# Kernel tuning notes

Measured on AMD Instinct MI355X. Metric: run time of the kernel, lower is better.

The kernel has to match this reference:

```python
import jax, jax.numpy as jnp
import numpy as np

C = 128          # channel_size
H = 2            # num_head
HD = C // H      # per-head dim = 64
SCALE = C ** 0.5 # note: module scales by sqrt(channel_size), not sqrt(head_dim)


def setup_inputs() -> dict:
    key = jax.random.key(0)
    k_x, k_w, k_b = jax.random.split(key, 3)
    x = jax.random.normal(k_x, (8, 64, 256, C), dtype=jnp.float32)
    # nn.Linear(C, 3C): weight [3C, C], bias [3C]; y = x @ W.T + b
    bound = 1.0 / np.sqrt(C)
    W_qkv = jax.random.uniform(k_w, (3 * C, C), dtype=jnp.float32, minval=-bound, maxval=bound)
    b_qkv = jax.random.uniform(k_b, (3 * C,), dtype=jnp.float32, minval=-bound, maxval=bound)
    return {"x": x, "W_qkv": W_qkv, "b_qkv": b_qkv}


def reference(x, W_qkv, b_qkv):
    b, l, g, _ = x.shape
    qkv = jnp.einsum('blgc,dc->blgd', x, W_qkv) + b_qkv        # [b,l,g,3C]
    # rearrange 'b l g (d h c) -> d b l h g c'
    qkv = qkv.reshape(b, l, g, 3, H, HD)
    qkv = jnp.transpose(qkv, (3, 0, 1, 4, 2, 5))               # [3,b,l,h,g,c]
    q, k, v = qkv[0], qkv[1], qkv[2]
    score = jnp.einsum('blhgc,blhkc->blhgk', q, k) / SCALE      # [b,l,h,g,g]
    score = jax.nn.softmax(score, axis=-1)
    out = jnp.einsum('blhgk,blhkc->blhgc', score, v)            # [b,l,h,g,c]
    # rearrange 'b l h g c -> b l g (h c)'
    out = jnp.transpose(out, (0, 1, 3, 2, 4)).reshape(b, l, g, H * HD)
    return out
```

## Files before the change

### kernel.cpp

```cpp
#include <hip/hip_runtime.h>
#include <hip/hip_bf16.h>


typedef __bf16 bf16x8 __attribute__((ext_vector_type(8)));
typedef float  f32x4  __attribute__((ext_vector_type(4)));
typedef float  f32x16 __attribute__((ext_vector_type(16)));

#define MFMA16(a, b, c) __builtin_amdgcn_mfma_f32_16x16x32_bf16((a), (b), (c), 0, 0, 0)
#define MFMA32(a, b, c) __builtin_amdgcn_mfma_f32_32x32x16_bf16((a), (b), (c), 0, 0, 0)

namespace dmsa {

constexpr int G  = 256;
constexpr int C  = 128;
constexpr int HD = 64;
constexpr float QSCALE = 1.4426950408889634f * 0.08838834764831845f;

__device__ __forceinline__ unsigned pack2(float a, float b) {
    union { __hip_bfloat162 h; unsigned u; } c;
    c.h = __float22bfloat162_rn(make_float2(a, b));
    return c.u;
}
__device__ __forceinline__ uint2 pack4(float a, float b, float c, float d) {
    uint2 r; r.x = pack2(a, b); r.y = pack2(c, d); return r;
}
__device__ __forceinline__ uint4 pack8(const float* p) {
    uint4 r;
    r.x = pack2(p[0], p[1]); r.y = pack2(p[2], p[3]);
    r.z = pack2(p[4], p[5]); r.w = pack2(p[6], p[7]);
    return r;
}
__device__ __forceinline__ bf16x8 lds8(const ushort* p) { return *(const bf16x8*)p; }
__device__ __forceinline__ bf16x8 ldg8(const ushort* p) { return *(const bf16x8*)p; }
__device__ __forceinline__ bf16x8 ld8f(const float* __restrict__ p) {
    float t[8];
    *(float4*)t       = *(const float4*)p;
    *(float4*)(t + 4) = *(const float4*)(p + 4);
    union { uint4 u; bf16x8 v; } c;
    c.u = pack8(t);
    return c.v;
}

__global__ void convw(const float* __restrict__ W, ushort* __restrict__ wbf) {
    int t = blockIdx.x * 256 + threadIdx.x;
    float tmp[8];
    const float* p = W + (size_t)t * 8;
    *(float4*)tmp       = *(const float4*)p;
    *(float4*)(tmp + 4) = *(const float4*)(p + 4);
    *(uint4*)(wbf + (size_t)t * 8) = pack8(tmp);
}

__global__ __launch_bounds__(256, 2)
void fused(const float* __restrict__ x, const ushort* __restrict__ wb,
           const float* __restrict__ bias, float* __restrict__ out)
{
    __shared__ ushort kc[G * 72];
    __shared__ ushort vc[HD * 264];

    const int tid = threadIdx.x, wv = tid >> 6, lane = tid & 63;
    const int l16 = lane & 15, quad = lane >> 4;
    const int l32 = lane & 31, hl = lane >> 5;

    const int b  = blockIdx.x;
    const int L  = ((b & 7) << 7) | (b >> 3);
    const int bl = L >> 1, h = L & 1;

    const float*  xr = x  + (size_t)bl * G * C;
    const ushort* Wq = wb + (size_t)(h * HD) * C;
    const ushort* Wk = wb + (size_t)(C + h * HD) * C;
    const ushort* Wv = wb + (size_t)(2 * C + h * HD) * C;

    const int r0 = wv * 64;
    const f32x4 z4 = {0.f, 0.f, 0.f, 0.f};

    bf16x8 xf[4][4];
    #pragma unroll
    for (int i = 0; i < 4; ++i)
        #pragma unroll
        for (int kk = 0; kk < 4; ++kk)
            xf[i][kk] = ld8f(xr + (size_t)(r0 + i * 16 + l16) * C + kk * 32 + quad * 8);

    f32x4 qacc[4][4];
    #pragma unroll
    for (int mi = 0; mi < 4; ++mi)
        #pragma unroll
        for (int ni = 0; ni < 4; ++ni) qacc[mi][ni] = z4;
    #pragma unroll
    for (int kk = 0; kk < 4; ++kk)
        #pragma unroll
        for (int mi = 0; mi < 4; ++mi) {
            bf16x8 a = ldg8(Wq + (size_t)(mi * 16 + l16) * C + kk * 32 + quad * 8);
            #pragma unroll
            for (int ni = 0; ni < 4; ++ni)
                qacc[mi][ni] = MFMA16(a, xf[ni][kk], qacc[mi][ni]);
        }
    ushort* qs = kc + r0 * 72;
    #pragma unroll
    for (int mi = 0; mi < 4; ++mi) {
        float4 bs = *(const float4*)(bias + h * HD + mi * 16 + quad * 4);
        #pragma unroll
        for (int ni = 0; ni < 4; ++ni)
            *(uint2*)(qs + (ni * 16 + l16) * 72 + mi * 16 + quad * 4) =
                pack4((qacc[mi][ni][0] + bs.x) * QSCALE,
                      (qacc[mi][ni][1] + bs.y) * QSCALE,
                      (qacc[mi][ni][2] + bs.z) * QSCALE,
                      (qacc[mi][ni][3] + bs.w) * QSCALE);
    }
    bf16x8 qf[2][4];
    #pragma unroll
    for (int ni = 0; ni < 2; ++ni)
        #pragma unroll
        for (int kk = 0; kk < 4; ++kk)
            qf[ni][kk] = lds8(qs + (ni * 32 + l32) * 72 + kk * 16 + hl * 8);

    {
        f32x4 kacc[4][4];
        #pragma unroll
        for (int mi = 0; mi < 4; ++mi)
            #pragma unroll
            for (int nt = 0; nt < 4; ++nt) kacc[mi][nt] = z4;
        #pragma unroll
        for (int kk = 0; kk < 4; ++kk)
            #pragma unroll
            for (int mi = 0; mi < 4; ++mi) {
                bf16x8 a = ldg8(Wk + (size_t)(mi * 16 + l16) * C + kk * 32 + quad * 8);
                #pragma unroll
                for (int nt = 0; nt < 4; ++nt)
                    kacc[mi][nt] = MFMA16(a, xf[nt][kk], kacc[mi][nt]);
            }
        #pragma unroll
        for (int mi = 0; mi < 4; ++mi) {
            float4 bs = *(const float4*)(bias + C + h * HD + mi * 16 + quad * 4);
            #pragma unroll
            for (int nt = 0; nt < 4; ++nt)
                *(uint2*)(kc + (r0 + nt * 16 + l16) * 72 + mi * 16 + quad * 4) =
                    pack4(kacc[mi][nt][0] + bs.x, kacc[mi][nt][1] + bs.y,
                          kacc[mi][nt][2] + bs.z, kacc[mi][nt][3] + bs.w);
        }
    }

    {
        f32x4 vacc[4][4];
        #pragma unroll
        for (int mt = 0; mt < 4; ++mt)
            #pragma unroll
            for (int nt = 0; nt < 4; ++nt) vacc[mt][nt] = z4;
        #pragma unroll
        for (int kk = 0; kk < 4; ++kk)
            #pragma unroll
            for (int nt = 0; nt < 4; ++nt) {
                bf16x8 bw = ldg8(Wv + (size_t)(nt * 16 + l16) * C + kk * 32 + quad * 8);
                #pragma unroll
                for (int mt = 0; mt < 4; ++mt)
                    vacc[mt][nt] = MFMA16(xf[mt][kk], bw, vacc[mt][nt]);
            }
        #pragma unroll
        for (int nt = 0; nt < 4; ++nt) {
            float bv = bias[2 * C + h * HD + nt * 16 + l16];
            #pragma unroll
            for (int mt = 0; mt < 4; ++mt)
                *(uint2*)(vc + (nt * 16 + l16) * 264 + r0 + mt * 16 + quad * 4) =
                    pack4(vacc[mt][nt][0] + bv, vacc[mt][nt][1] + bv,
                          vacc[mt][nt][2] + bv, vacc[mt][nt][3] + bv);
        }
    }

    __syncthreads();

    float lacc[2] = {0.f, 0.f};
    f32x16 oacc[2][2];
    #pragma unroll
    for (int mt = 0; mt < 2; ++mt)
        #pragma unroll
        for (int ni = 0; ni < 2; ++ni)
            #pragma unroll
            for (int r = 0; r < 16; ++r) oacc[mt][ni][r] = 0.f;

    #pragma unroll 2
    for (int sp = 0; sp < 8; ++sp) {
        const int g0 = sp * 32;

        bf16x8 kf[4];
        #pragma unroll
        for (int kk = 0; kk < 4; ++kk)
            kf[kk] = lds8(kc + (g0 + l32) * 72 + kk * 16 + hl * 8);
        bf16x8 vf[2][2];
        #pragma unroll
        for (int mt = 0; mt < 2; ++mt)
            #pragma unroll
            for (int ch = 0; ch < 2; ++ch)
                vf[mt][ch] = lds8(vc + (mt * 32 + l32) * 264 + g0 + ch * 16 + hl * 8);

        #pragma unroll
        for (int ni = 0; ni < 2; ++ni) {
            f32x16 s;
            #pragma unroll
            for (int r = 0; r < 16; ++r) s[r] = 0.f;
            __builtin_amdgcn_s_setprio(1);
            #pragma unroll
            for (int kk = 0; kk < 4; ++kk)
                s = MFMA32(kf[kk], qf[ni][kk], s);
            __builtin_amdgcn_s_setprio(0);

            float part = 0.f;
            #pragma unroll
            for (int r = 0; r < 16; ++r) {
                float p = exp2f(s[r]);
                s[r] = p;
                part += p;
            }
            lacc[ni] += part;

            #pragma unroll
            for (int ch = 0; ch < 2; ++ch) {
                unsigned p0a = pack2(s[8 * ch + 0], s[8 * ch + 1]);
                unsigned p0b = pack2(s[8 * ch + 2], s[8 * ch + 3]);
                unsigned p1a = pack2(s[8 * ch + 4], s[8 * ch + 5]);
                unsigned p1b = pack2(s[8 * ch + 6], s[8 * ch + 7]);
                auto w02 = __builtin_amdgcn_permlane32_swap((int)p0a, (int)p1a, false, false);
                auto w13 = __builtin_amdgcn_permlane32_swap((int)p0b, (int)p1b, false, false);
                union { uint4 u; bf16x8 v; } pf;
                pf.u.x = (unsigned)w02[0]; pf.u.y = (unsigned)w13[0];
                pf.u.z = (unsigned)w02[1]; pf.u.w = (unsigned)w13[1];
                __builtin_amdgcn_s_setprio(1);
                #pragma unroll
                for (int mt = 0; mt < 2; ++mt)
                    oacc[mt][ni] = MFMA32(vf[mt][ch], pf.v, oacc[mt][ni]);
                __builtin_amdgcn_s_setprio(0);
            }
        }
    }

    float* og = out + (size_t)bl * G * C + h * HD;
    #pragma unroll
    for (int ni = 0; ni < 2; ++ni) {
        float l = lacc[ni];
        l += __shfl_xor(l, 32);
        float inv = 1.0f / l;
        int g = r0 + ni * 32 + l32;
        #pragma unroll
        for (int mt = 0; mt < 2; ++mt)
            #pragma unroll
            for (int rr = 0; rr < 4; ++rr) {
                float4 st;
                st.x = oacc[mt][ni][4 * rr + 0] * inv;
                st.y = oacc[mt][ni][4 * rr + 1] * inv;
                st.z = oacc[mt][ni][4 * rr + 2] * inv;
                st.w = oacc[mt][ni][4 * rr + 3] * inv;
                *(float4*)(og + (size_t)g * C + mt * 32 + rr * 8 + hl * 4) = st;
            }
    }
}

}

extern "C" void kernel_launch(void* const* d_in, const int* in_sizes, int n_in,
                              void* d_out, int out_size, void* d_ws, size_t ws_size,
                              hipStream_t stream) {
    (void)in_sizes; (void)n_in; (void)out_size;

    if (ws_size < (size_t)384 * 128 * 2) return;

    const float* x    = (const float*)d_in[0];
    const float* W    = (const float*)d_in[1];
    const float* bias = (const float*)d_in[2];
    float* out = (float*)d_out;

    ushort* wbf = (ushort*)d_ws;

    dmsa::convw<<<dim3(24),   dim3(256), 0, stream>>>(W, wbf);
    dmsa::fused<<<dim3(1024), dim3(256), 0, stream>>>(x, wbf, bias, out);
}
```

Baseline: 166.1 us.

## Split each block's work across eight waves instead of four

Each block now runs 512 threads, so every wave owns 32 query rows instead of 64. Per-wave register arrays for the projections and attention shrink, which allows more resident waves for latency hiding (launch bounds 512,4). The cost is that each wave reloads the full Wq/Wk/Wv tiles from global memory for half as much work, doubling total weight-fetch traffic. The key and value fragments read from LDS in the attention loop are also amortised over fewer queries, doubling total LDS reads.

```diff
diff --git a/kernel.cpp b/kernel.cpp
--- a/kernel.cpp
+++ b/kernel.cpp
@@ -50,7 +50,7 @@
     *(uint4*)(wbf + (size_t)t * 8) = pack8(tmp);
 }
 
-__global__ __launch_bounds__(256, 2)
+__global__ __launch_bounds__(512, 4)
 void fused(const float* __restrict__ x, const ushort* __restrict__ wb,
            const float* __restrict__ bias, float* __restrict__ out)
 {
@@ -70,28 +70,28 @@
     const ushort* Wk = wb + (size_t)(C + h * HD) * C;
     const ushort* Wv = wb + (size_t)(2 * C + h * HD) * C;
 
-    const int r0 = wv * 64;
+    const int r0 = wv * 32;
     const f32x4 z4 = {0.f, 0.f, 0.f, 0.f};
 
-    bf16x8 xf[4][4];
-    #pragma unroll
-    for (int i = 0; i < 4; ++i)
+    bf16x8 xf[2][4];
+    #pragma unroll
+    for (int i = 0; i < 2; ++i)
         #pragma unroll
         for (int kk = 0; kk < 4; ++kk)
             xf[i][kk] = ld8f(xr + (size_t)(r0 + i * 16 + l16) * C + kk * 32 + quad * 8);
 
-    f32x4 qacc[4][4];
+    f32x4 qacc[4][2];
     #pragma unroll
     for (int mi = 0; mi < 4; ++mi)
         #pragma unroll
-        for (int ni = 0; ni < 4; ++ni) qacc[mi][ni] = z4;
+        for (int ni = 0; ni < 2; ++ni) qacc[mi][ni] = z4;
     #pragma unroll
     for (int kk = 0; kk < 4; ++kk)
         #pragma unroll
         for (int mi = 0; mi < 4; ++mi) {
             bf16x8 a = ldg8(Wq + (size_t)(mi * 16 + l16) * C + kk * 32 + quad * 8);
             #pragma unroll
-            for (int ni = 0; ni < 4; ++ni)
+            for (int ni = 0; ni < 2; ++ni)
                 qacc[mi][ni] = MFMA16(a, xf[ni][kk], qacc[mi][ni]);
         }
     ushort* qs = kc + r0 * 72;
@@ -99,40 +99,38 @@
     for (int mi = 0; mi < 4; ++mi) {
         float4 bs = *(const float4*)(bias + h * HD + mi * 16 + quad * 4);
         #pragma unroll
-        for (int ni = 0; ni < 4; ++ni)
+        for (int ni = 0; ni < 2; ++ni)
             *(uint2*)(qs + (ni * 16 + l16) * 72 + mi * 16 + quad * 4) =
                 pack4((qacc[mi][ni][0] + bs.x) * QSCALE,
                       (qacc[mi][ni][1] + bs.y) * QSCALE,
                       (qacc[mi][ni][2] + bs.z) * QSCALE,
                       (qacc[mi][ni][3] + bs.w) * QSCALE);
     }
-    bf16x8 qf[2][4];
-    #pragma unroll
-    for (int ni = 0; ni < 2; ++ni)
-        #pragma unroll
-        for (int kk = 0; kk < 4; ++kk)
-            qf[ni][kk] = lds8(qs + (ni * 32 + l32) * 72 + kk * 16 + hl * 8);
+    bf16x8 qf[4];
+    #pragma unroll
+    for (int kk = 0; kk < 4; ++kk)
+        qf[kk] = lds8(qs + l32 * 72 + kk * 16 + hl * 8);
 
     {
-        f32x4 kacc[4][4];
+        f32x4 kacc[4][2];
         #pragma unroll
         for (int mi = 0; mi < 4; ++mi)
             #pragma unroll
-            for (int nt = 0; nt < 4; ++nt) kacc[mi][nt] = z4;
+            for (int nt = 0; nt < 2; ++nt) kacc[mi][nt] = z4;
         #pragma unroll
         for (int kk = 0; kk < 4; ++kk)
             #pragma unroll
             for (int mi = 0; mi < 4; ++mi) {
                 bf16x8 a = ldg8(Wk + (size_t)(mi * 16 + l16) * C + kk * 32 + quad * 8);
                 #pragma unroll
-                for (int nt = 0; nt < 4; ++nt)
+                for (int nt = 0; nt < 2; ++nt)
                     kacc[mi][nt] = MFMA16(a, xf[nt][kk], kacc[mi][nt]);
             }
         #pragma unroll
         for (int mi = 0; mi < 4; ++mi) {
             float4 bs = *(const float4*)(bias + C + h * HD + mi * 16 + quad * 4);
             #pragma unroll
-            for (int nt = 0; nt < 4; ++nt)
+            for (int nt = 0; nt < 2; ++nt)
                 *(uint2*)(kc + (r0 + nt * 16 + l16) * 72 + mi * 16 + quad * 4) =
                     pack4(kacc[mi][nt][0] + bs.x, kacc[mi][nt][1] + bs.y,
                           kacc[mi][nt][2] + bs.z, kacc[mi][nt][3] + bs.w);
@@ -140,9 +138,9 @@
     }
 
     {
-        f32x4 vacc[4][4];
-        #pragma unroll
-        for (int mt = 0; mt < 4; ++mt)
+        f32x4 vacc[2][4];
+        #pragma unroll
+        for (int mt = 0; mt < 2; ++mt)
             #pragma unroll
             for (int nt = 0; nt < 4; ++nt) vacc[mt][nt] = z4;
         #pragma unroll
@@ -151,14 +149,14 @@
             for (int nt = 0; nt < 4; ++nt) {
                 bf16x8 bw = ldg8(Wv + (size_t)(nt * 16 + l16) * C + kk * 32 + quad * 8);
                 #pragma unroll
-                for (int mt = 0; mt < 4; ++mt)
+                for (int mt = 0; mt < 2; ++mt)
                     vacc[mt][nt] = MFMA16(xf[mt][kk], bw, vacc[mt][nt]);
             }
         #pragma unroll
         for (int nt = 0; nt < 4; ++nt) {
             float bv = bias[2 * C + h * HD + nt * 16 + l16];
             #pragma unroll
-            for (int mt = 0; mt < 4; ++mt)
+            for (int mt = 0; mt < 2; ++mt)
                 *(uint2*)(vc + (nt * 16 + l16) * 264 + r0 + mt * 16 + quad * 4) =
                     pack4(vacc[mt][nt][0] + bv, vacc[mt][nt][1] + bv,
                           vacc[mt][nt][2] + bv, vacc[mt][nt][3] + bv);
@@ -167,14 +165,12 @@
 
     __syncthreads();
 
-    float lacc[2] = {0.f, 0.f};
-    f32x16 oacc[2][2];
+    float lacc = 0.f;
+    f32x16 oacc[2];
     #pragma unroll
     for (int mt = 0; mt < 2; ++mt)
         #pragma unroll
-        for (int ni = 0; ni < 2; ++ni)
-            #pragma unroll
-            for (int r = 0; r < 16; ++r) oacc[mt][ni][r] = 0.f;
+        for (int r = 0; r < 16; ++r) oacc[mt][r] = 0.f;
 
     #pragma unroll 2
     for (int sp = 0; sp < 8; ++sp) {
@@ -191,62 +187,58 @@
             for (int ch = 0; ch < 2; ++ch)
                 vf[mt][ch] = lds8(vc + (mt * 32 + l32) * 264 + g0 + ch * 16 + hl * 8);
 
-        #pragma unroll
-        for (int ni = 0; ni < 2; ++ni) {
-            f32x16 s;
-            #pragma unroll
-            for (int r = 0; r < 16; ++r) s[r] = 0.f;
+        f32x16 s;
+        #pragma unroll
+        for (int r = 0; r < 16; ++r) s[r] = 0.f;
+        __builtin_amdgcn_s_setprio(1);
+        #pragma unroll
+        for (int kk = 0; kk < 4; ++kk)
+            s = MFMA32(kf[kk], qf[kk], s);
+        __builtin_amdgcn_s_setprio(0);
+
+        float part = 0.f;
+        #pragma unroll
+        for (int r = 0; r < 16; ++r) {
+            float p = exp2f(s[r]);
+            s[r] = p;
+            part += p;
+        }
+        lacc += part;
+
+        #pragma unroll
+        for (int ch = 0; ch < 2; ++ch) {
+            unsigned p0a = pack2(s[8 * ch + 0], s[8 * ch + 1]);
+            unsigned p0b = pack2(s[8 * ch + 2], s[8 * ch + 3]);
+            unsigned p1a = pack2(s[8 * ch + 4], s[8 * ch + 5]);
+            unsigned p1b = pack2(s[8 * ch + 6], s[8 * ch + 7]);
+            auto w02 = __builtin_amdgcn_permlane32_swap((int)p0a, (int)p1a, false, false);
+            auto w13 = __builtin_amdgcn_permlane32_swap((int)p0b, (int)p1b, false, false);
+            union { uint4 u; bf16x8 v; } pf;
+            pf.u.x = (unsigned)w02[0]; pf.u.y = (unsigned)w13[0];
+            pf.u.z = (unsigned)w02[1]; pf.u.w = (unsigned)w13[1];
             __builtin_amdgcn_s_setprio(1);
             #pragma unroll
-            for (int kk = 0; kk < 4; ++kk)
-                s = MFMA32(kf[kk], qf[ni][kk], s);
+            for (int mt = 0; mt < 2; ++mt)
+                oacc[mt] = MFMA32(vf[mt][ch], pf.v, oacc[mt]);
             __builtin_amdgcn_s_setprio(0);
-
-            float part = 0.f;
-            #pragma unroll
-            for (int r = 0; r < 16; ++r) {
-                float p = exp2f(s[r]);
-                s[r] = p;
-                part += p;
-            }
-            lacc[ni] += part;
-
-            #pragma unroll
-            for (int ch = 0; ch < 2; ++ch) {
-                unsigned p0a = pack2(s[8 * ch + 0], s[8 * ch + 1]);
-                unsigned p0b = pack2(s[8 * ch + 2], s[8 * ch + 3]);
-                unsigned p1a = pack2(s[8 * ch + 4], s[8 * ch + 5]);
-                unsigned p1b = pack2(s[8 * ch + 6], s[8 * ch + 7]);
-                auto w02 = __builtin_amdgcn_permlane32_swap((int)p0a, (int)p1a, false, false);
-                auto w13 = __builtin_amdgcn_permlane32_swap((int)p0b, (int)p1b, false, false);
-                union { uint4 u; bf16x8 v; } pf;
-                pf.u.x = (unsigned)w02[0]; pf.u.y = (unsigned)w13[0];
-                pf.u.z = (unsigned)w02[1]; pf.u.w = (unsigned)w13[1];
-                __builtin_amdgcn_s_setprio(1);
-                #pragma unroll
-                for (int mt = 0; mt < 2; ++mt)
-                    oacc[mt][ni] = MFMA32(vf[mt][ch], pf.v, oacc[mt][ni]);
-                __builtin_amdgcn_s_setprio(0);
-            }
         }
     }
 
     float* og = out + (size_t)bl * G * C + h * HD;
-    #pragma unroll
-    for (int ni = 0; ni < 2; ++ni) {
-        float l = lacc[ni];
+    {
+        float l = lacc;
         l += __shfl_xor(l, 32);
         float inv = 1.0f / l;
-        int g = r0 + ni * 32 + l32;
+        int g = r0 + l32;
         #pragma unroll
         for (int mt = 0; mt < 2; ++mt)
             #pragma unroll
             for (int rr = 0; rr < 4; ++rr) {
                 float4 st;
-                st.x = oacc[mt][ni][4 * rr + 0] * inv;
-                st.y = oacc[mt][ni][4 * rr + 1] * inv;
-                st.z = oacc[mt][ni][4 * rr + 2] * inv;
-                st.w = oacc[mt][ni][4 * rr + 3] * inv;
+                st.x = oacc[mt][4 * rr + 0] * inv;
+                st.y = oacc[mt][4 * rr + 1] * inv;
+                st.z = oacc[mt][4 * rr + 2] * inv;
+                st.w = oacc[mt][4 * rr + 3] * inv;
                 *(float4*)(og + (size_t)g * C + mt * 32 + rr * 8 + hl * 4) = st;
             }
     }
@@ -269,5 +261,5 @@
     ushort* wbf = (ushort*)d_ws;
 
     dmsa::convw<<<dim3(24),   dim3(256), 0, stream>>>(W, wbf);
-    dmsa::fused<<<dim3(1024), dim3(256), 0, stream>>>(x, wbf, bias, out);
-}
+    dmsa::fused<<<dim3(1024), dim3(512), 0, stream>>>(x, wbf, bias, out);
+}
```

After: 186.8 us. 12.5% more time.
